# Kernel tuning notes

Measured on AMD Instinct MI355X. Metric: run time of the kernel, lower is better.

Reference implementation:

```python
import jax, jax.numpy as jnp
import numpy as np

NUM_STRINGS = 6
WEIGHT_FRET_ONSET = 0.5
STRING_WEIGHTS = jnp.ones((NUM_STRINGS,), dtype=jnp.float32)

B, S, T, C = 64, 6, 2000, 25


def setup_inputs() -> dict:
    key = jax.random.key(0)
    k1, k2, k3, k4 = jax.random.split(key, 4)
    return {
        "output_fret": jax.random.normal(k1, (B, S, T, C), dtype=jnp.float32),
        "target_fret": jax.random.randint(k2, (B, S, T), 0, C),
        "output_onset": jax.random.normal(k3, (B, S, T), dtype=jnp.float32),
        "target_onset": jax.random.uniform(k4, (B, S, T), dtype=jnp.float32),
    }


def reference(output_fret, target_fret, output_onset, target_onset):
    # ---- fret loss: standard CE over classes, mean over batch per (s,t),
    #      summed over frames, weighted per string ----
    logp_fret = jax.nn.log_softmax(output_fret, axis=-1)            # [B,S,T,C]
    nll = -jnp.take_along_axis(logp_fret, target_fret[..., None], axis=-1)[..., 0]  # [B,S,T]
    fret_st = nll.mean(axis=0)                                       # [S,T] (reduction='mean' over batch)
    fret_string_losses = fret_st.sum(axis=1) * STRING_WEIGHTS        # [S]
    fret_loss = fret_string_losses.sum()

    # ---- onset loss: torch CE with 1D [B] input + [B] float target =
    #      single example with B classes and probability targets:
    #      softmax over the BATCH dimension ----
    logp_on = jax.nn.log_softmax(output_onset, axis=0)               # softmax over B
    on_st = -(target_onset * logp_on).sum(axis=0)                    # [S,T]
    onset_string_losses = on_st.sum(axis=1) * STRING_WEIGHTS         # [S]
    onset_loss = onset_string_losses.sum()

    loss = WEIGHT_FRET_ONSET * fret_loss + (1.0 - WEIGHT_FRET_ONSET) * onset_loss
    return (loss, fret_loss, onset_loss, fret_string_losses, onset_string_losses)
```

## Files before the change

### kernel.cpp

```cpp
#include <hip/hip_runtime.h>
#include <math.h>

constexpr int Bn = 64, Sn = 6, Tn = 2000, Cn = 25;
constexpr int COLS = Sn * Tn;
constexpr int ROWS = Bn * Sn * Tn;
constexpr int BDIM = 256;
constexpr int WV   = 4;

constexpr int RPB  = 256;
constexpr int TF4  = RPB * Cn / 4;
constexpr int FBLK = ROWS / RPB;
constexpr int FPAD = 3072;

constexpr int OCOLS = 64;
constexpr int OBLK  = (COLS + OCOLS - 1) / OCOLS;
constexpr int OPAD  = 192;
constexpr int GRID  = OBLK + FBLK;

static __device__ __forceinline__ void seg_reduce_add(float* ls, int s, float v, int lane) {
    const int s0 = __shfl(s, 0, 64);
    const int s1 = __shfl(s, 63, 64);
    if (s0 == s1) {
        float a = v;
        #pragma unroll
        for (int off = 32; off; off >>= 1) a += __shfl_xor(a, off, 64);
        if (lane == 0) atomicAdd(&ls[s0], a);
    } else {
        float a = (s == s0) ? v : 0.0f;
        float b = (s == s0) ? 0.0f : v;
        #pragma unroll
        for (int off = 32; off; off >>= 1) {
            a += __shfl_xor(a, off, 64);
            b += __shfl_xor(b, off, 64);
        }
        if (lane == 0) { atomicAdd(&ls[s0], a); atomicAdd(&ls[s1], b); }
    }
}

__global__ __launch_bounds__(BDIM) void main_kernel(const float4* __restrict__ x4,
                                                    const int*    __restrict__ tgt,
                                                    const float*  __restrict__ ox,
                                                    const float*  __restrict__ ot,
                                                    float* __restrict__ pf,
                                                    float* __restrict__ po) {
    __shared__ float lds[RPB * Cn];
    __shared__ float ws[WV][Sn];
    const int tid  = threadIdx.x;
    const int lane = tid & 63;
    const int w    = tid >> 6;
    if (lane < Sn) ws[w][lane] = 0.0f;

    if (blockIdx.x < OBLK) {
        const int cb  = blockIdx.x;
        const int col = cb * OCOLS + lane;
        float4* ob4 = (float4*)lds;
        float M = -INFINITY, S = 0.0f, ts = 0.0f, txs = 0.0f;
        if (col < COLS) {
            const int b0 = w * 16;
            #pragma unroll
            for (int h = 0; h < 2; ++h) {
                float xv[8], tv[8];
                #pragma unroll
                for (int k = 0; k < 8; ++k) xv[k] = ox[(b0 + h * 8 + k) * COLS + col];
                #pragma unroll
                for (int k = 0; k < 8; ++k) tv[k] = ot[(b0 + h * 8 + k) * COLS + col];
                float cm = -INFINITY;
                #pragma unroll
                for (int k = 0; k < 8; ++k) cm = fmaxf(cm, xv[k]);
                float cs = 0.0f;
                #pragma unroll
                for (int k = 0; k < 8; ++k) cs += __expf(xv[k] - cm);
                const float nm = fmaxf(M, cm);
                S = S * __expf(M - nm) + cs * __expf(cm - nm);
                M = nm;
                #pragma unroll
                for (int k = 0; k < 8; ++k) { ts += tv[k]; txs += tv[k] * xv[k]; }
            }
        }
        ob4[w * OCOLS + lane] = make_float4(M, S, ts, txs);
        __syncthreads();
        if (tid < OCOLS) {
            float on = 0.0f;
            int   s  = Sn - 1;
            const int c = cb * OCOLS + tid;
            if (c < COLS) {
                s = c / Tn;
                float4 p0 = ob4[0 * OCOLS + tid];
                float Mm = p0.x, Sm = p0.y, tsm = p0.z, txm = p0.w;
                #pragma unroll
                for (int q = 1; q < WV; ++q) {
                    const float4 p = ob4[q * OCOLS + tid];
                    const float nm = fmaxf(Mm, p.x);
                    Sm  = Sm * __expf(Mm - nm) + p.y * __expf(p.x - nm);
                    Mm  = nm;
                    tsm += p.z; txm += p.w;
                }
                on = tsm * (Mm + __logf(Sm)) - txm;
            }
            seg_reduce_add(ws[0], s, on, tid);
            if (tid < Sn) po[tid * OPAD + cb] = ws[0][tid];
        }
    } else {
        const int fb  = blockIdx.x - OBLK;
        const int row = fb * RPB + tid;
        const int tc  = tgt[row];
        const float4* src = x4 + (long)fb * TF4;
        float4* lds4 = (float4*)lds;
        #pragma unroll
        for (int k = tid; k < TF4; k += BDIM) lds4[k] = src[k];
        __syncthreads();

        const float* rp = lds + tid * Cn;
        float m = -INFINITY, xt = 0.0f;
        #pragma unroll
        for (int c = 0; c < Cn; ++c) {
            const float e = rp[c];
            m  = fmaxf(m, e);
            xt = (c == tc) ? e : xt;
        }
        float ss = 0.0f;
        #pragma unroll
        for (int c = 0; c < Cn; ++c) ss += __expf(rp[c] - m);
        const float nll = m + __logf(ss) - xt;

        const int s = (row / Tn) % Sn;
        seg_reduce_add(ws[w], s, nll, lane);
        __syncthreads();
        if (tid < Sn)
            pf[tid * FPAD + fb] = ws[0][tid] + ws[1][tid] + ws[2][tid] + ws[3][tid];
    }
}

__global__ __launch_bounds__(1024) void finish_kernel(const float* __restrict__ pf,
                                                      const float* __restrict__ po,
                                                      float* __restrict__ out) {
    __shared__ float acc[2 * Sn];
    const int tid  = threadIdx.x;
    const int lane = tid & 63;
    if (tid < 2 * Sn) acc[tid] = 0.0f;
    __syncthreads();

    float fs[Sn];
    #pragma unroll
    for (int s = 0; s < Sn; ++s) {
        float v = 0.0f;
        for (int i = tid; i < FBLK; i += 1024) v += pf[s * FPAD + i];
        fs[s] = v;
    }
    #pragma unroll
    for (int off = 32; off; off >>= 1) {
        #pragma unroll
        for (int s = 0; s < Sn; ++s) fs[s] += __shfl_xor(fs[s], off, 64);
    }
    if (lane == 0) {
        #pragma unroll
        for (int s = 0; s < Sn; ++s) atomicAdd(&acc[s], fs[s]);
    }

    const int wv = tid >> 6;
    if (wv < Sn) {
        float v = 0.0f;
        for (int i = lane; i < OBLK; i += 64) v += po[wv * OPAD + i];
        #pragma unroll
        for (int off = 32; off; off >>= 1) v += __shfl_xor(v, off, 64);
        if (lane == 0) acc[Sn + wv] = v;
    }
    __syncthreads();

    if (tid == 0) {
        float fret = 0.0f, on = 0.0f, fsv[Sn], osv[Sn];
        #pragma unroll
        for (int s = 0; s < Sn; ++s) {
            fsv[s] = acc[s] * (1.0f / Bn);
            osv[s] = acc[Sn + s];
            fret += fsv[s];
            on   += osv[s];
        }
        out[0] = 0.5f * fret + 0.5f * on;
        out[1] = fret;
        out[2] = on;
        #pragma unroll
        for (int s = 0; s < Sn; ++s) { out[3 + s] = fsv[s]; out[9 + s] = osv[s]; }
    }
}

extern "C" void kernel_launch(void* const* d_in, const int* in_sizes, int n_in,
                              void* d_out, int out_size, void* d_ws, size_t ws_size,
                              hipStream_t stream) {
    const float* output_fret  = (const float*)d_in[0];
    const int*   target_fret  = (const int*)d_in[1];
    const float* output_onset = (const float*)d_in[2];
    const float* target_onset = (const float*)d_in[3];
    float* pf  = (float*)d_ws;
    float* po  = pf + Sn * FPAD;
    float* out = (float*)d_out;

    main_kernel<<<GRID, BDIM, 0, stream>>>((const float4*)output_fret, target_fret,
                                           output_onset, target_onset, pf, po);
    finish_kernel<<<1, 1024, 0, stream>>>(pf, po, out);
}
```

Measured before the change: 29.73 us.

## Double-buffer per-wave fret tiles with direct global-to-LDS async loads

The fret branch is restructured so each wave processes four 64-row tiles, staging them into a private double buffer with global_load_lds. The next tile's load overlaps compute on the current one, and block-wide synchronisation before compute is dropped. Each block now covers four times more rows, so the grid shrinks and fewer partials go to the finish kernel. The manual vmcnt/lgkmcnt waits are fragile, and the larger per-block work may reduce parallelism.

```diff
diff --git a/kernel.cpp b/kernel.cpp
--- a/kernel.cpp
+++ b/kernel.cpp
@@ -7,15 +7,21 @@
 constexpr int BDIM = 256;
 constexpr int WV   = 4;
 
-constexpr int RPB  = 256;
-constexpr int TF4  = RPB * Cn / 4;
-constexpr int FBLK = ROWS / RPB;
-constexpr int FPAD = 3072;
+constexpr int TROWS = 64;
+constexpr int TF4   = TROWS * Cn / 4;
+constexpr int NT    = 4;
+constexpr int RPW   = NT * TROWS;
+constexpr int RPB   = WV * RPW;
+constexpr int FBLK  = ROWS / RPB;
+constexpr int FPAD  = 768;
 
 constexpr int OCOLS = 64;
 constexpr int OBLK  = (COLS + OCOLS - 1) / OCOLS;
 constexpr int OPAD  = 192;
 constexpr int GRID  = OBLK + FBLK;
+
+typedef const __attribute__((address_space(1))) unsigned int guint;
+typedef __attribute__((address_space(3)))       unsigned int luint;
 
 static __device__ __forceinline__ void seg_reduce_add(float* ls, int s, float v, int lane) {
     const int s0 = __shfl(s, 0, 64);
@@ -43,8 +49,8 @@
                                                     const float*  __restrict__ ot,
                                                     float* __restrict__ pf,
                                                     float* __restrict__ po) {
-    __shared__ float lds[RPB * Cn];
-    __shared__ float ws[WV][Sn];
+    __shared__ float4 buf4[WV][2][TF4];
+    __shared__ float  ws[WV][Sn];
     const int tid  = threadIdx.x;
     const int lane = tid & 63;
     const int w    = tid >> 6;
@@ -53,7 +59,7 @@
     if (blockIdx.x < OBLK) {
         const int cb  = blockIdx.x;
         const int col = cb * OCOLS + lane;
-        float4* ob4 = (float4*)lds;
+        float4* ob4 = &buf4[0][0][0];
         float M = -INFINITY, S = 0.0f, ts = 0.0f, txs = 0.0f;
         if (col < COLS) {
             const int b0 = w * 16;
@@ -101,30 +107,60 @@
             if (tid < Sn) po[tid * OPAD + cb] = ws[0][tid];
         }
     } else {
-        const int fb  = blockIdx.x - OBLK;
-        const int row = fb * RPB + tid;
-        const int tc  = tgt[row];
-        const float4* src = x4 + (long)fb * TF4;
-        float4* lds4 = (float4*)lds;
-        #pragma unroll
-        for (int k = tid; k < TF4; k += BDIM) lds4[k] = src[k];
-        __syncthreads();
-
-        const float* rp = lds + tid * Cn;
-        float m = -INFINITY, xt = 0.0f;
-        #pragma unroll
-        for (int c = 0; c < Cn; ++c) {
-            const float e = rp[c];
-            m  = fmaxf(m, e);
-            xt = (c == tc) ? e : xt;
-        }
-        float ss = 0.0f;
-        #pragma unroll
-        for (int c = 0; c < Cn; ++c) ss += __expf(rp[c] - m);
-        const float nll = m + __logf(ss) - xt;
-
-        const int s = (row / Tn) % Sn;
-        seg_reduce_add(ws[w], s, nll, lane);
+        const int fb    = blockIdx.x - OBLK;
+        const int wrow0 = fb * RPB + w * RPW;
+        const float4* gw = x4 + (long)(wrow0 / 4) * Cn;
+        float4* bb = &buf4[w][0][0];
+
+        int tcs[NT];
+        #pragma unroll
+        for (int t = 0; t < NT; ++t) tcs[t] = tgt[wrow0 + t * TROWS + lane];
+
+        auto stage = [&](int t) {
+            const int b = t & 1;
+            const float4* gs = gw + (long)t * TF4 + lane;
+            #pragma unroll
+            for (int k = 0; k < 6; ++k)
+                __builtin_amdgcn_global_load_lds((guint*)(gs + k * 64),
+                                                 (luint*)(bb + b * TF4 + k * 64), 16, 0, 0);
+            if (lane < 16)
+                __builtin_amdgcn_global_load_lds((guint*)(gs + 384),
+                                                 (luint*)(bb + b * TF4 + 384), 16, 0, 0);
+        };
+
+        auto compute = [&](int t) {
+            const int b  = t & 1;
+            const int tc = tcs[t];
+            const float* rp = (const float*)(bb + b * TF4) + lane * Cn;
+            float m = -INFINITY, xt = 0.0f;
+            #pragma unroll
+            for (int c = 0; c < Cn; ++c) {
+                const float e = rp[c];
+                m  = fmaxf(m, e);
+                xt = (c == tc) ? e : xt;
+            }
+            float ss = 0.0f;
+            #pragma unroll
+            for (int c = 0; c < Cn; ++c) ss += __expf(rp[c] - m);
+            const float nll = m + __logf(ss) - xt;
+            const int s = ((wrow0 + t * TROWS + lane) / Tn) % Sn;
+            seg_reduce_add(ws[w], s, nll, lane);
+        };
+
+        stage(0);
+        stage(1);
+        #pragma unroll
+        for (int t = 0; t < NT; ++t) {
+            if (t < NT - 1)
+                asm volatile("s_waitcnt vmcnt(7)" ::: "memory");
+            else
+                asm volatile("s_waitcnt vmcnt(0)" ::: "memory");
+            compute(t);
+            if (t + 2 < NT) {
+                asm volatile("s_waitcnt lgkmcnt(0)" ::: "memory");
+                stage(t + 2);
+            }
+        }
         __syncthreads();
         if (tid < Sn)
             pf[tid * FPAD + fb] = ws[0][tid] + ws[1][tid] + ws[2][tid] + ws[3][tid];
```

New measurement: 25.94 us. -12.7%, faster.
